# Kernel optimization log

Hardware: AMD Instinct MI355X
Metric: run time of the kernel (lower is better)

## Reference

```python
import jax, jax.numpy as jnp
import numpy as np

NT, NGRID, NX, HID, NY = 365, 1000, 20, 256, 1


def setup_inputs() -> dict:
    key = jax.random.key(0)
    ks = jax.random.split(key, 10)
    s_in = 1.0 / np.sqrt(NX)
    s_h = 1.0 / np.sqrt(HID)
    inp = {
        "x": jax.random.normal(ks[0], (NT, NGRID, NX), dtype=jnp.float32),
        "wt_ih": jnp.zeros((4 * HID, HID), dtype=jnp.float32),
        "W_in": jax.random.uniform(ks[1], (HID, NX), jnp.float32, -s_in, s_in),
        "b_in": jax.random.uniform(ks[2], (HID,), jnp.float32, -s_in, s_in),
        "W_ih": jax.random.uniform(ks[3], (4 * HID, HID), jnp.float32, -s_h, s_h),
        "W_hh": jax.random.uniform(ks[4], (4 * HID, HID), jnp.float32, -s_h, s_h),
        "b_ih": jax.random.uniform(ks[5], (4 * HID,), jnp.float32, -s_h, s_h),
        "b_hh": jax.random.uniform(ks[6], (4 * HID,), jnp.float32, -s_h, s_h),
        "W_out": jax.random.uniform(ks[7], (NY, HID), jnp.float32, -s_h, s_h),
        "b_out": jax.random.uniform(ks[8], (NY,), jnp.float32, -s_h, s_h),
    }
    return inp


def _lstm_forward(x, W_in, b_in, W_ih, W_hh, b_ih, b_hh, W_out, b_out):
    # linearIn + ReLU: [nt, ngrid, hid]
    x0 = jax.nn.relu(jnp.einsum("tnx,hx->tnh", x, W_in) + b_in)
    # precompute input contribution to gates for all timesteps: [nt, ngrid, 4*hid]
    gx = jnp.einsum("tnh,gh->tng", x0, W_ih) + b_ih + b_hh
    h0 = jnp.zeros((x.shape[1], HID), dtype=x.dtype)
    c0 = jnp.zeros((x.shape[1], HID), dtype=x.dtype)

    def step(carry, gx_t):
        h, c = carry
        gates = gx_t + h @ W_hh.T  # [ngrid, 4*hid]
        i, f, g, o = jnp.split(gates, 4, axis=-1)  # torch LSTMCell gate order
        i = jax.nn.sigmoid(i)
        f = jax.nn.sigmoid(f)
        g = jnp.tanh(g)
        o = jax.nn.sigmoid(o)
        c_new = f * c + i * g
        h_new = o * jnp.tanh(c_new)
        return (h_new, c_new), h_new

    _, hs = jax.lax.scan(step, (h0, c0), gx)  # hs: [nt, ngrid, hid]
    return jnp.einsum("tnh,yh->tny", hs, W_out) + b_out


def reference(x, wt_ih, W_in, b_in, W_ih, W_hh, b_ih, b_hh, W_out, b_out):
    # wt_ih only perturbs weights in training mode (and is zero here); eval-mode math:
    return _lstm_forward(x, W_in, b_in, W_ih, W_hh, b_ih, b_hh, W_out, b_out)
```

## Files before the change

kernel.cpp:

```cpp
#include <hip/hip_runtime.h>
#include <hip/hip_fp16.h>

#define NT    365
#define NGRID 1000
#define NXI   20
#define HID   256
#define GATES 1024
#define MROWS 365000
#define MBLK  5704
#define MPAD  (MBLK * 64)
#define NCL   63
#define CPTS  16
#define HX_TOT ((size_t)NT * NCL * 1024)
#define HX_ZERO ((size_t)NCL * 1024)

typedef _Float16 half8 __attribute__((ext_vector_type(8)));
typedef float floatx4 __attribute__((ext_vector_type(4)));
typedef unsigned long long u64;

#define SENT 0xFFFFFFFFFFFFFFFFull

__device__ _Float16 g_gx[(size_t)MPAD * GATES];
__device__ _Float16 g_wif[64 * 8 * 512];
__device__ _Float16 g_whf[2 * 32 * 8 * 64 * 8];
__device__ u64 g_hx[HX_TOT];

__device__ __forceinline__ float fsig(float x) {
  return __fdividef(1.f, 1.f + __expf(-x));
}
__device__ __forceinline__ float ftanh(float x) {
  return 1.f - __fdividef(2.f, __expf(2.f * x) + 1.f);
}

__global__ __launch_bounds__(256) void init_kernel(float* __restrict__ y) {
  const size_t i = (size_t)blockIdx.x * 256 + threadIdx.x;
  const size_t j = i * 2;
  if (j < HX_TOT)     g_hx[j]     = (j < HX_ZERO)     ? 0ull : SENT;
  if (j + 1 < HX_TOT) g_hx[j + 1] = (j + 1 < HX_ZERO) ? 0ull : SENT;
  if (i < MROWS) y[i] = 0.f;
}

__global__ __launch_bounds__(256) void pack_wf_kernel(
    const float* __restrict__ W_ih, const float* __restrict__ W_hh) {
  const int gid = blockIdx.x * 256 + threadIdx.x;
  const float* src;
  _Float16* dst;
  int n, k0, lane;
  if (gid < 32768) {
    const int tile = gid >> 9;
    const int ks   = (gid >> 6) & 7;
    lane = gid & 63;
    n  = tile * 16 + (lane & 15);
    k0 = ks * 32 + (lane >> 4) * 8;
    src = W_ih + n * HID + k0;
    dst = g_wif + ((size_t)(tile * 8 + ks) * 64 + lane) * 8;
  } else {
    const int rem = gid - 32768;
    const int b2  = rem >> 14;
    const int lt  = (rem >> 9) & 31;
    const int ks  = (rem >> 6) & 7;
    lane = rem & 63;
    const int nt = (lt >> 3) * 16 + b2 * 8 + (lt & 7);
    n  = nt * 16 + (lane & 15);
    k0 = ks * 32 + (lane >> 4) * 8;
    src = W_hh + n * HID + k0;
    dst = g_whf + ((size_t)((b2 * 32 + lt) * 8 + ks) * 64 + lane) * 8;
  }
  const float4 a = *(const float4*)(src);
  const float4 b = *(const float4*)(src + 4);
  half8 h;
  h[0] = (_Float16)a.x; h[1] = (_Float16)a.y; h[2] = (_Float16)a.z; h[3] = (_Float16)a.w;
  h[4] = (_Float16)b.x; h[5] = (_Float16)b.y; h[6] = (_Float16)b.z; h[7] = (_Float16)b.w;
  *(half8*)dst = h;
}

__global__ __launch_bounds__(256, 2) void gx_kernel(
    const float* __restrict__ x, const float* __restrict__ W_in,
    const float* __restrict__ b_in, const float* __restrict__ b_ih,
    const float* __restrict__ b_hh) {
  __shared__ float s_x[64 * NXI];
  __shared__ _Float16 s_x0[64 * 264];
  __shared__ _Float16 s_out[64 * 264];

  const int tid  = threadIdx.x;
  const int lane = tid & 63;
  const int w    = tid >> 6;
  const int m0   = blockIdx.x * 64;

  #pragma unroll
  for (int i = 0; i < 5; ++i) {
    const int idx = i * 256 + tid;
    size_t g = (size_t)m0 * NXI + idx;
    const size_t gmax = (size_t)MROWS * NXI - 1;
    if (g > gmax) g = gmax;
    s_x[idx] = x[g];
  }
  float wv[NXI];
  #pragma unroll
  for (int k = 0; k < NXI; ++k) wv[k] = W_in[tid * NXI + k];
  const float bv = b_in[tid];
  __syncthreads();

  for (int r = 0; r < 64; ++r) {
    float acc = bv;
    #pragma unroll
    for (int qq = 0; qq < 5; ++qq) {
      const float4 xa = *(const float4*)&s_x[r * NXI + qq * 4];
      acc += xa.x * wv[qq * 4 + 0] + xa.y * wv[qq * 4 + 1] +
             xa.z * wv[qq * 4 + 2] + xa.w * wv[qq * 4 + 3];
    }
    s_x0[r * 264 + tid] = (_Float16)fmaxf(acc, 0.f);
  }
  __syncthreads();

  for (int ng = 0; ng < 4; ++ng) {
    floatx4 acc[4][4];
    #pragma unroll
    for (int mi = 0; mi < 4; ++mi)
      #pragma unroll
      for (int ni = 0; ni < 4; ++ni) acc[mi][ni] = (floatx4){0.f, 0.f, 0.f, 0.f};

    #pragma unroll
    for (int ks = 0; ks < 8; ++ks) {
      half8 a[4], bfr[4];
      #pragma unroll
      for (int mi = 0; mi < 4; ++mi)
        a[mi] = *(const half8*)&s_x0[(mi * 16 + (lane & 15)) * 264 + ks * 32 + (lane >> 4) * 8];
      #pragma unroll
      for (int ni = 0; ni < 4; ++ni) {
        const int nt = ng * 16 + w * 4 + ni;
        bfr[ni] = *(const half8*)(g_wif + ((size_t)(nt * 8 + ks) * 64 + lane) * 8);
      }
      #pragma unroll
      for (int mi = 0; mi < 4; ++mi)
        #pragma unroll
        for (int ni = 0; ni < 4; ++ni)
          acc[mi][ni] = __builtin_amdgcn_mfma_f32_16x16x32_f16(a[mi], bfr[ni], acc[mi][ni], 0, 0, 0);
    }

    #pragma unroll
    for (int ni = 0; ni < 4; ++ni) {
      const int g = ng * 256 + (w * 4 + ni) * 16 + (lane & 15);
      const float bias = b_ih[g] + b_hh[g];
      const int colw = (w * 4 + ni) * 16 + (lane & 15);
      #pragma unroll
      for (int mi = 0; mi < 4; ++mi)
        #pragma unroll
        for (int r = 0; r < 4; ++r)
          s_out[(mi * 16 + (lane >> 4) * 4 + r) * 264 + colw] = (_Float16)(acc[mi][ni][r] + bias);
    }
    __syncthreads();

    #pragma unroll
    for (int i = 0; i < 8; ++i) {
      const int cid = i * 256 + tid;
      const int row = cid >> 5;
      const int c8  = (cid & 31) * 8;
      const half8 v = *(const half8*)&s_out[row * 264 + c8];
      const int phi = ((c8 >> 7) & 1) * 512 + ng * 128 + (c8 & 127);
      *(half8*)(g_gx + (size_t)(m0 + row) * GATES + phi) = v;
    }
    __syncthreads();
  }
}

__global__ __launch_bounds__(256, 1) void rec_kernel(
    const float* __restrict__ W_out, const float* __restrict__ b_out,
    float* __restrict__ y) {
  __shared__ float s_g[4 * 16 * 132];
  __shared__ u64   s_h[2][1024];

  const int tid = threadIdx.x;
  const int l   = tid & 63;
  const int w   = tid >> 6;
  const int c   = blockIdx.x >> 1;
  const int b   = blockIdx.x & 1;
  const int pt  = l & 15;
  const int jg  = l >> 4;

  half8 wf[8][8];
  #pragma unroll
  for (int slot = 0; slot < 8; ++slot) {
    const int lt = (slot >> 1) * 8 + 2 * w + (slot & 1);
    #pragma unroll
    for (int kk = 0; kk < 4; ++kk) {
      wf[slot][kk] = *(const half8*)(g_whf +
          ((size_t)((b * 32 + lt) * 8 + (b * 4 + kk)) * 64 + l) * 8);
      wf[slot][4 + kk] = *(const half8*)(g_whf +
          ((size_t)((b * 32 + lt) * 8 + ((1 - b) * 4 + kk)) * 64 + l) * 8);
    }
  }

  float cs[8];
  float wo[8];
  #pragma unroll
  for (int j = 0; j < 8; ++j) {
    cs[j] = 0.f;
    wo[j] = W_out[b * 128 + 32 * w + jg * 8 + j];
  }
  const float bo_eff = (b == 0 && w == 0) ? b_out[0] : 0.f;
  const int n_pt  = c * CPTS + pt;
  const int rn_pt = (n_pt < NGRID) ? n_pt : (NGRID - 1);
  const int peer0 = (1 - b) * 4;

  for (int i = tid; i < 1024; i += 256) s_h[0][i] = 0ull;
  __syncthreads();

  for (int t = 0; t < NT; ++t) {
    const int cur = t & 1, nxt = cur ^ 1;

    half8 gxr[4];
    {
      const _Float16* gsrc = g_gx + ((size_t)t * NGRID + rn_pt) * GATES
                           + b * 512 + 32 * w + jg * 8;
      #pragma unroll
      for (int off = 0; off < 4; ++off)
        gxr[off] = *(const half8*)(gsrc + off * 128);
    }

    const u64* hsrc = g_hx + ((size_t)t * NCL + c) * 1024;
    u64 pv[8];
    #pragma unroll
    for (int kk = 0; kk < 4; ++kk) {
      pv[2 * kk]     = __hip_atomic_load(hsrc +       (peer0 + kk) * 64 + l,
                                         __ATOMIC_RELAXED, __HIP_MEMORY_SCOPE_AGENT);
      pv[2 * kk + 1] = __hip_atomic_load(hsrc + 512 + (peer0 + kk) * 64 + l,
                                         __ATOMIC_RELAXED, __HIP_MEMORY_SCOPE_AGENT);
    }

    floatx4 acc[8];
    #pragma unroll
    for (int i = 0; i < 8; ++i) acc[i] = (floatx4){0.f, 0.f, 0.f, 0.f};

    #pragma unroll
    for (int kk = 0; kk < 4; ++kk) {
      union { u64 u[2]; half8 h; } af;
      af.u[0] = s_h[cur][kk * 64 + l];
      af.u[1] = s_h[cur][512 + kk * 64 + l];
      #pragma unroll
      for (int i = 0; i < 8; ++i)
        acc[i] = __builtin_amdgcn_mfma_f32_16x16x32_f16(af.h, wf[i][kk], acc[i], 0, 0, 0);
    }

    {
      bool pending = false;
      #pragma unroll
      for (int k = 0; k < 8; ++k) pending |= (pv[k] == SENT);
      int tries = 0;
      while (pending && ++tries < (1 << 18)) {
        pending = false;
        #pragma unroll
        for (int kk = 0; kk < 4; ++kk) {
          if (pv[2 * kk] == SENT)
            pv[2 * kk] = __hip_atomic_load(hsrc + (peer0 + kk) * 64 + l,
                                           __ATOMIC_RELAXED, __HIP_MEMORY_SCOPE_AGENT);
          if (pv[2 * kk + 1] == SENT)
            pv[2 * kk + 1] = __hip_atomic_load(hsrc + 512 + (peer0 + kk) * 64 + l,
                                               __ATOMIC_RELAXED, __HIP_MEMORY_SCOPE_AGENT);
        }
        #pragma unroll
        for (int k = 0; k < 8; ++k) pending |= (pv[k] == SENT);
      }
    }

    #pragma unroll
    for (int kk = 0; kk < 4; ++kk) {
      union { u64 u[2]; half8 h; } af;
      af.u[0] = pv[2 * kk];
      af.u[1] = pv[2 * kk + 1];
      #pragma unroll
      for (int i = 0; i < 8; ++i)
        acc[i] = __builtin_amdgcn_mfma_f32_16x16x32_f16(af.h, wf[i][4 + kk], acc[i], 0, 0, 0);
    }

    #pragma unroll
    for (int slot = 0; slot < 8; ++slot) {
      const int colw = (slot >> 1) * 32 + (slot & 1) * 16 + pt;
      #pragma unroll
      for (int r = 0; r < 4; ++r)
        s_g[w * 2112 + (jg * 4 + r) * 132 + colw] = acc[slot][r];
    }

    {
      const float* gp = &s_g[w * 2112 + pt * 132 + jg * 8];
      union { u64 u[2]; _Float16 h[8]; } pub;
      float yp = 0.f;
      #pragma unroll
      for (int j = 0; j < 8; ++j) {
        const float gi = gp[j]      + (float)gxr[0][j];
        const float gf = gp[32 + j] + (float)gxr[1][j];
        const float gg = gp[64 + j] + (float)gxr[2][j];
        const float go = gp[96 + j] + (float)gxr[3][j];
        const float i_ = fsig(gi);
        const float f_ = fsig(gf);
        const float g_ = ftanh(gg);
        const float o_ = fsig(go);
        cs[j] = f_ * cs[j] + i_ * g_;
        const float h = o_ * ftanh(cs[j]);
        pub.h[j] = (_Float16)h;
        yp += wo[j] * h;
      }
      if (t < NT - 1) {
        u64* dst = g_hx + ((size_t)(t + 1) * NCL + c) * 1024 + (b * 4 + w) * 64 + l;
        __hip_atomic_store(dst,       pub.u[0], __ATOMIC_RELAXED, __HIP_MEMORY_SCOPE_AGENT);
        __hip_atomic_store(dst + 512, pub.u[1], __ATOMIC_RELAXED, __HIP_MEMORY_SCOPE_AGENT);
      }
      s_h[nxt][w * 64 + l]       = pub.u[0];
      s_h[nxt][512 + w * 64 + l] = pub.u[1];
      yp += __shfl_xor(yp, 16);
      yp += __shfl_xor(yp, 32);
      if (jg == 0 && n_pt < NGRID)
        atomicAdd(&y[(size_t)t * NGRID + n_pt], yp + bo_eff);
    }
    __syncthreads();
  }
}

extern "C" void kernel_launch(void* const* d_in, const int* in_sizes, int n_in,
                              void* d_out, int out_size, void* d_ws, size_t ws_size,
                              hipStream_t stream) {
  (void)in_sizes; (void)n_in; (void)out_size; (void)d_ws; (void)ws_size;
  const float* x     = (const float*)d_in[0];
  const float* W_in  = (const float*)d_in[2];
  const float* b_in  = (const float*)d_in[3];
  const float* W_ih  = (const float*)d_in[4];
  const float* W_hh  = (const float*)d_in[5];
  const float* b_ih  = (const float*)d_in[6];
  const float* b_hh  = (const float*)d_in[7];
  const float* W_out = (const float*)d_in[8];
  const float* b_out = (const float*)d_in[9];
  float* y           = (float*)d_out;

  const int init_blocks = (int)((HX_TOT / 2 + 255) / 256);
  hipLaunchKernelGGL(init_kernel, dim3(init_blocks), dim3(256), 0, stream, y);
  hipLaunchKernelGGL(pack_wf_kernel, dim3(256), dim3(256), 0, stream, W_ih, W_hh);
  hipLaunchKernelGGL(gx_kernel, dim3(MBLK), dim3(256), 0, stream,
                     x, W_in, b_in, b_ih, b_hh);
  hipLaunchKernelGGL(rec_kernel, dim3(NCL * 2), dim3(256), 0, stream, W_out, b_out, y);
}
```

Baseline: 1.858 ms.

## Drop LDS h exchange and block barrier; exchange hidden state per-wave via global

Each wave now keeps only its own h slice in registers and fetches the other seven k-slices (including sibling waves in the same block) from the global sentinel buffer, removing the shared-memory h double buffer and the per-step __syncthreads. Global loads for the next step's h and gx are issued right after publishing, so they overlap the output reduction. In exchange each wave polls more global data per step and depends on L2 latency for intra-block peers; the spin limit is also halved.

```diff
diff --git a/kernel.cpp b/kernel.cpp
--- a/kernel.cpp
+++ b/kernel.cpp
@@ -19,6 +19,8 @@
 typedef unsigned long long u64;
 
 #define SENT 0xFFFFFFFFFFFFFFFFull
+
+union hpack { u64 u[2]; half8 h; _Float16 e[8]; };
 
 __device__ _Float16 g_gx[(size_t)MPAD * GATES];
 __device__ _Float16 g_wif[64 * 8 * 512];
@@ -168,7 +170,6 @@
     const float* __restrict__ W_out, const float* __restrict__ b_out,
     float* __restrict__ y) {
   __shared__ float s_g[4 * 16 * 132];
-  __shared__ u64   s_h[2][1024];
 
   const int tid = threadIdx.x;
   const int l   = tid & 63;
@@ -178,17 +179,21 @@
   const int pt  = l & 15;
   const int jg  = l >> 4;
 
+  const int kown = b * 4 + w;
+  int ko[7];
+  #pragma unroll
+  for (int s = 0; s < 7; ++s) ko[s] = s + (s >= kown ? 1 : 0);
+
   half8 wf[8][8];
   #pragma unroll
-  for (int slot = 0; slot < 8; ++slot) {
-    const int lt = (slot >> 1) * 8 + 2 * w + (slot & 1);
-    #pragma unroll
-    for (int kk = 0; kk < 4; ++kk) {
-      wf[slot][kk] = *(const half8*)(g_whf +
-          ((size_t)((b * 32 + lt) * 8 + (b * 4 + kk)) * 64 + l) * 8);
-      wf[slot][4 + kk] = *(const half8*)(g_whf +
-          ((size_t)((b * 32 + lt) * 8 + ((1 - b) * 4 + kk)) * 64 + l) * 8);
-    }
+  for (int i = 0; i < 8; ++i) {
+    const int lt = (i >> 1) * 8 + 2 * w + (i & 1);
+    #pragma unroll
+    for (int s = 0; s < 7; ++s)
+      wf[i][s] = *(const half8*)(g_whf +
+          ((size_t)((b * 32 + lt) * 8 + ko[s]) * 64 + l) * 8);
+    wf[i][7] = *(const half8*)(g_whf +
+        ((size_t)((b * 32 + lt) * 8 + kown) * 64 + l) * 8);
   }
 
   float cs[8];
@@ -201,89 +206,81 @@
   const float bo_eff = (b == 0 && w == 0) ? b_out[0] : 0.f;
   const int n_pt  = c * CPTS + pt;
   const int rn_pt = (n_pt < NGRID) ? n_pt : (NGRID - 1);
-  const int peer0 = (1 - b) * 4;
-
-  for (int i = tid; i < 1024; i += 256) s_h[0][i] = 0ull;
-  __syncthreads();
+
+  hpack pubPrev;
+  pubPrev.u[0] = 0ull; pubPrev.u[1] = 0ull;
+
+  u64 pv[14];
+  {
+    const u64* hsrc = g_hx + (size_t)c * 1024;
+    #pragma unroll
+    for (int s = 0; s < 7; ++s) {
+      pv[2 * s]     = __hip_atomic_load(hsrc +       ko[s] * 64 + l,
+                                        __ATOMIC_RELAXED, __HIP_MEMORY_SCOPE_AGENT);
+      pv[2 * s + 1] = __hip_atomic_load(hsrc + 512 + ko[s] * 64 + l,
+                                        __ATOMIC_RELAXED, __HIP_MEMORY_SCOPE_AGENT);
+    }
+  }
+  half8 gxr[4];
+  {
+    const _Float16* gsrc = g_gx + (size_t)rn_pt * GATES + b * 512 + 32 * w + jg * 8;
+    #pragma unroll
+    for (int off = 0; off < 4; ++off) gxr[off] = *(const half8*)(gsrc + off * 128);
+  }
 
   for (int t = 0; t < NT; ++t) {
-    const int cur = t & 1, nxt = cur ^ 1;
-
-    half8 gxr[4];
-    {
-      const _Float16* gsrc = g_gx + ((size_t)t * NGRID + rn_pt) * GATES
-                           + b * 512 + 32 * w + jg * 8;
-      #pragma unroll
-      for (int off = 0; off < 4; ++off)
-        gxr[off] = *(const half8*)(gsrc + off * 128);
-    }
-
     const u64* hsrc = g_hx + ((size_t)t * NCL + c) * 1024;
-    u64 pv[8];
-    #pragma unroll
-    for (int kk = 0; kk < 4; ++kk) {
-      pv[2 * kk]     = __hip_atomic_load(hsrc +       (peer0 + kk) * 64 + l,
-                                         __ATOMIC_RELAXED, __HIP_MEMORY_SCOPE_AGENT);
-      pv[2 * kk + 1] = __hip_atomic_load(hsrc + 512 + (peer0 + kk) * 64 + l,
-                                         __ATOMIC_RELAXED, __HIP_MEMORY_SCOPE_AGENT);
-    }
 
     floatx4 acc[8];
     #pragma unroll
     for (int i = 0; i < 8; ++i) acc[i] = (floatx4){0.f, 0.f, 0.f, 0.f};
 
     #pragma unroll
-    for (int kk = 0; kk < 4; ++kk) {
-      union { u64 u[2]; half8 h; } af;
-      af.u[0] = s_h[cur][kk * 64 + l];
-      af.u[1] = s_h[cur][512 + kk * 64 + l];
-      #pragma unroll
-      for (int i = 0; i < 8; ++i)
-        acc[i] = __builtin_amdgcn_mfma_f32_16x16x32_f16(af.h, wf[i][kk], acc[i], 0, 0, 0);
-    }
+    for (int i = 0; i < 8; ++i)
+      acc[i] = __builtin_amdgcn_mfma_f32_16x16x32_f16(pubPrev.h, wf[i][7], acc[i], 0, 0, 0);
 
     {
       bool pending = false;
       #pragma unroll
-      for (int k = 0; k < 8; ++k) pending |= (pv[k] == SENT);
+      for (int k = 0; k < 14; ++k) pending |= (pv[k] == SENT);
       int tries = 0;
-      while (pending && ++tries < (1 << 18)) {
+      while (pending && ++tries < (1 << 17)) {
+        #pragma unroll
+        for (int s = 0; s < 7; ++s) {
+          if (pv[2 * s] == SENT)
+            pv[2 * s] = __hip_atomic_load(hsrc + ko[s] * 64 + l,
+                                          __ATOMIC_RELAXED, __HIP_MEMORY_SCOPE_AGENT);
+          if (pv[2 * s + 1] == SENT)
+            pv[2 * s + 1] = __hip_atomic_load(hsrc + 512 + ko[s] * 64 + l,
+                                              __ATOMIC_RELAXED, __HIP_MEMORY_SCOPE_AGENT);
+        }
         pending = false;
         #pragma unroll
-        for (int kk = 0; kk < 4; ++kk) {
-          if (pv[2 * kk] == SENT)
-            pv[2 * kk] = __hip_atomic_load(hsrc + (peer0 + kk) * 64 + l,
-                                           __ATOMIC_RELAXED, __HIP_MEMORY_SCOPE_AGENT);
-          if (pv[2 * kk + 1] == SENT)
-            pv[2 * kk + 1] = __hip_atomic_load(hsrc + 512 + (peer0 + kk) * 64 + l,
-                                               __ATOMIC_RELAXED, __HIP_MEMORY_SCOPE_AGENT);
-        }
-        #pragma unroll
-        for (int k = 0; k < 8; ++k) pending |= (pv[k] == SENT);
+        for (int k = 0; k < 14; ++k) pending |= (pv[k] == SENT);
       }
     }
 
     #pragma unroll
-    for (int kk = 0; kk < 4; ++kk) {
-      union { u64 u[2]; half8 h; } af;
-      af.u[0] = pv[2 * kk];
-      af.u[1] = pv[2 * kk + 1];
+    for (int s = 0; s < 7; ++s) {
+      hpack af;
+      af.u[0] = pv[2 * s];
+      af.u[1] = pv[2 * s + 1];
       #pragma unroll
       for (int i = 0; i < 8; ++i)
-        acc[i] = __builtin_amdgcn_mfma_f32_16x16x32_f16(af.h, wf[i][4 + kk], acc[i], 0, 0, 0);
-    }
-
-    #pragma unroll
-    for (int slot = 0; slot < 8; ++slot) {
-      const int colw = (slot >> 1) * 32 + (slot & 1) * 16 + pt;
+        acc[i] = __builtin_amdgcn_mfma_f32_16x16x32_f16(af.h, wf[i][s], acc[i], 0, 0, 0);
+    }
+
+    #pragma unroll
+    for (int i = 0; i < 8; ++i) {
+      const int colw = (i >> 1) * 32 + (i & 1) * 16 + pt;
       #pragma unroll
       for (int r = 0; r < 4; ++r)
-        s_g[w * 2112 + (jg * 4 + r) * 132 + colw] = acc[slot][r];
+        s_g[w * 2112 + (jg * 4 + r) * 132 + colw] = acc[i][r];
     }
 
     {
       const float* gp = &s_g[w * 2112 + pt * 132 + jg * 8];
-      union { u64 u[2]; _Float16 h[8]; } pub;
+      hpack pub;
       float yp = 0.f;
       #pragma unroll
       for (int j = 0; j < 8; ++j) {
@@ -297,22 +294,37 @@
         const float o_ = fsig(go);
         cs[j] = f_ * cs[j] + i_ * g_;
         const float h = o_ * ftanh(cs[j]);
-        pub.h[j] = (_Float16)h;
+        pub.e[j] = (_Float16)h;
         yp += wo[j] * h;
       }
+
       if (t < NT - 1) {
-        u64* dst = g_hx + ((size_t)(t + 1) * NCL + c) * 1024 + (b * 4 + w) * 64 + l;
+        u64* dst = g_hx + ((size_t)(t + 1) * NCL + c) * 1024 + kown * 64 + l;
         __hip_atomic_store(dst,       pub.u[0], __ATOMIC_RELAXED, __HIP_MEMORY_SCOPE_AGENT);
         __hip_atomic_store(dst + 512, pub.u[1], __ATOMIC_RELAXED, __HIP_MEMORY_SCOPE_AGENT);
+
+        const u64* hn = g_hx + ((size_t)(t + 1) * NCL + c) * 1024;
+        #pragma unroll
+        for (int s = 0; s < 7; ++s) {
+          pv[2 * s]     = __hip_atomic_load(hn +       ko[s] * 64 + l,
+                                            __ATOMIC_RELAXED, __HIP_MEMORY_SCOPE_AGENT);
+          pv[2 * s + 1] = __hip_atomic_load(hn + 512 + ko[s] * 64 + l,
+                                            __ATOMIC_RELAXED, __HIP_MEMORY_SCOPE_AGENT);
+        }
       }
-      s_h[nxt][w * 64 + l]       = pub.u[0];
-      s_h[nxt][512 + w * 64 + l] = pub.u[1];
+      pubPrev = pub;
+
       yp += __shfl_xor(yp, 16);
       yp += __shfl_xor(yp, 32);
       if (jg == 0 && n_pt < NGRID)
         atomicAdd(&y[(size_t)t * NGRID + n_pt], yp + bo_eff);
-    }
-    __syncthreads();
+
+      const int tn = (t + 1 < NT) ? (t + 1) : t;
+      const _Float16* gsrc = g_gx + ((size_t)tn * NGRID + rn_pt) * GATES
+                           + b * 512 + 32 * w + jg * 8;
+      #pragma unroll
+      for (int off = 0; off < 4; ++off) gxr[off] = *(const half8*)(gsrc + off * 128);
+    }
   }
 }
 
```

After: 2.443 ms. 31.5% more time.
